# Kernel tuning notes

Hardware: AMD Instinct MI355X
Metric: run time of the kernel (lower is better)

Reference implementation:

```python
import jax, jax.numpy as jnp
import numpy as np

KSIZE = 3
RES_SCALE = 0.2
WITH_RESIDUAL = True


def setup_inputs() -> dict:
    key = jax.random.key(0)
    x = jax.random.normal(key, (8, 3, 1024, 1024), dtype=jnp.float32)
    return {"x": x}


def reference(x) -> jnp.ndarray:
    B, C, H, W = x.shape
    k = KSIZE
    p = k // 2
    # zero padding matches F.unfold(padding=k//2)
    xp = jnp.pad(x, ((0, 0), (0, 0), (p, p), (p, p)))
    # [B, C, k*k, H, W] stack of shifted views (k*k = 9, small static loop)
    patches = jnp.stack(
        [xp[:, :, di:di + H, dj:dj + W] for di in range(k) for dj in range(k)],
        axis=2,
    )
    # median of odd-sized window = middle element of sorted values
    med = jnp.sort(patches, axis=2)[:, :, (k * k) // 2]
    if WITH_RESIDUAL:
        return x + RES_SCALE * (med - x)
    return med
```

## Files before the change

kernel.cpp:

```cpp
#include <hip/hip_runtime.h>


#define S2(a, b) { float _t = fminf(a, b); b = fmaxf(a, b); a = _t; }

__device__ __forceinline__ float med3f(float a, float b, float c) {
    return fmaxf(fminf(a, b), fminf(fmaxf(a, b), c));
}

constexpr int ROWS = 16;

__global__ __launch_bounds__(256) void median_blur_kernel(
    const float* __restrict__ xin, float* __restrict__ out)
{
    const int W = 1024, H = 1024;
    const int tx   = threadIdx.x;
    const int lane = tx & 63;
    const int x0   = tx << 2;
    const int y0   = blockIdx.x * ROWS;
    const int z    = blockIdx.y;
    const size_t plane = (size_t)z * H * W;
    const float* base  = xin + plane;
    float*       obase = out + plane;

    float t[6], m[6], b[6];

    auto load_row = [&](int y, float* dst) {
        if (y < 0 || y >= H) {
#pragma unroll
            for (int j = 0; j < 6; ++j) dst[j] = 0.0f;
            return;
        }
        const float* row = base + (size_t)y * W;
        float4 c = *reinterpret_cast<const float4*>(row + x0);
        float left  = __shfl_up(c.w, 1);
        float right = __shfl_down(c.x, 1);
        if (lane == 0)  left  = (x0 > 0)     ? row[x0 - 1] : 0.0f;
        if (lane == 63) right = (x0 + 4 < W) ? row[x0 + 4] : 0.0f;
        dst[0] = left; dst[1] = c.x; dst[2] = c.y; dst[3] = c.z; dst[4] = c.w; dst[5] = right;
    };

    load_row(y0 - 1, t);
    load_row(y0,     m);
    load_row(y0 + 1, b);

#pragma unroll 4
    for (int r = 0; r < ROWS; ++r) {
        float nxt[6];
        {
            const int yn = (r < ROWS - 1) ? (y0 + r + 2) : H;
            load_row(yn, nxt);
        }

        float lo[6], mi[6], hi[6];
#pragma unroll
        for (int j = 0; j < 6; ++j) {
            float a = t[j], c0 = m[j], d = b[j];
            S2(a, c0); S2(c0, d); S2(a, c0);
            lo[j] = a; mi[j] = c0; hi[j] = d;
        }

        float4 o; float* op = &o.x;
#pragma unroll
        for (int j = 0; j < 4; ++j) {
            float mxlo = fmaxf(lo[j], fmaxf(lo[j + 1], lo[j + 2]));
            float mnhi = fminf(hi[j], fminf(hi[j + 1], hi[j + 2]));
            float mdmi = med3f(mi[j], mi[j + 1], mi[j + 2]);
            float med  = med3f(mxlo, mdmi, mnhi);
            float xc   = m[j + 1];
            op[j] = xc + 0.2f * (med - xc);
        }
        *reinterpret_cast<float4*>(obase + (size_t)(y0 + r) * W + x0) = o;

#pragma unroll
        for (int j = 0; j < 6; ++j) { t[j] = m[j]; m[j] = b[j]; b[j] = nxt[j]; }
    }
}

extern "C" void kernel_launch(void* const* d_in, const int* in_sizes, int n_in,
                              void* d_out, int out_size, void* d_ws, size_t ws_size,
                              hipStream_t stream) {
    const float* x = (const float*)d_in[0];
    float* out = (float*)d_out;
    const int H = 1024, W = 1024;
    const int planes = in_sizes[0] / (H * W);
    dim3 block(256);
    dim3 grid(H / ROWS, planes);
    median_blur_kernel<<<grid, block, 0, stream>>>(x, out);
}
```

Measured before the change: 182.1 us.

## Deepen row prefetch and load halo columns directly instead of shuffles

Raises the row prefetch distance from one to three rows ahead, keeping five rows in registers and fully unrolling the row loop. The left and right halo columns are now loaded directly from global memory (clamped and zero-masked), replacing the wavefront shuffles. Launch bounds now request four blocks per multiprocessor. The aim is to hide more memory latency in a bandwidth-bound stencil, at the cost of extra registers and redundant cached halo loads.

```diff
diff --git a/kernel.cpp b/kernel.cpp
--- a/kernel.cpp
+++ b/kernel.cpp
@@ -9,52 +9,58 @@
 
 constexpr int ROWS = 16;
 
-__global__ __launch_bounds__(256) void median_blur_kernel(
+struct Row { float v[6]; };
+
+__global__ __launch_bounds__(256, 4) void median_blur_kernel(
     const float* __restrict__ xin, float* __restrict__ out)
 {
     const int W = 1024, H = 1024;
-    const int tx   = threadIdx.x;
-    const int lane = tx & 63;
-    const int x0   = tx << 2;
-    const int y0   = blockIdx.x * ROWS;
-    const int z    = blockIdx.y;
-    const size_t plane = (size_t)z * H * W;
+    const int tx = threadIdx.x;
+    const int x0 = tx << 2;
+    const int y0 = blockIdx.x * ROWS;
+    const size_t plane = (size_t)blockIdx.y * H * W;
     const float* base  = xin + plane;
     float*       obase = out + plane;
 
-    float t[6], m[6], b[6];
+    const int  xl = (x0 > 0)     ? x0 - 1 : 0;
+    const int  xr = (x0 + 4 < W) ? x0 + 4 : W - 1;
+    const bool lz = (x0 == 0);
+    const bool rz = (x0 + 4 >= W);
 
-    auto load_row = [&](int y, float* dst) {
-        if (y < 0 || y >= H) {
+    auto load_row = [&](int y, Row& d) {
+        if ((unsigned)y < (unsigned)H) {
+            const float* row = base + (size_t)y * W;
+            const float4 c = *reinterpret_cast<const float4*>(row + x0);
+            const float  l = row[xl];
+            const float  r = row[xr];
+            d.v[0] = lz ? 0.0f : l;
+            d.v[1] = c.x; d.v[2] = c.y; d.v[3] = c.z; d.v[4] = c.w;
+            d.v[5] = rz ? 0.0f : r;
+        } else {
 #pragma unroll
-            for (int j = 0; j < 6; ++j) dst[j] = 0.0f;
-            return;
+            for (int j = 0; j < 6; ++j) d.v[j] = 0.0f;
         }
-        const float* row = base + (size_t)y * W;
-        float4 c = *reinterpret_cast<const float4*>(row + x0);
-        float left  = __shfl_up(c.w, 1);
-        float right = __shfl_down(c.x, 1);
-        if (lane == 0)  left  = (x0 > 0)     ? row[x0 - 1] : 0.0f;
-        if (lane == 63) right = (x0 + 4 < W) ? row[x0 + 4] : 0.0f;
-        dst[0] = left; dst[1] = c.x; dst[2] = c.y; dst[3] = c.z; dst[4] = c.w; dst[5] = right;
     };
 
+    Row t, m, b, p0, p1;
     load_row(y0 - 1, t);
     load_row(y0,     m);
     load_row(y0 + 1, b);
+    load_row(y0 + 2, p0);
+    load_row(y0 + 3, p1);
 
-#pragma unroll 4
+#pragma unroll
     for (int r = 0; r < ROWS; ++r) {
-        float nxt[6];
+        Row nx;
         {
-            const int yn = (r < ROWS - 1) ? (y0 + r + 2) : H;
-            load_row(yn, nxt);
+            const int yn = (r <= ROWS - 4) ? (y0 + r + 4) : H;
+            load_row(yn, nx);
         }
 
         float lo[6], mi[6], hi[6];
 #pragma unroll
         for (int j = 0; j < 6; ++j) {
-            float a = t[j], c0 = m[j], d = b[j];
+            float a = t.v[j], c0 = m.v[j], d = b.v[j];
             S2(a, c0); S2(c0, d); S2(a, c0);
             lo[j] = a; mi[j] = c0; hi[j] = d;
         }
@@ -66,13 +72,12 @@
             float mnhi = fminf(hi[j], fminf(hi[j + 1], hi[j + 2]));
             float mdmi = med3f(mi[j], mi[j + 1], mi[j + 2]);
             float med  = med3f(mxlo, mdmi, mnhi);
-            float xc   = m[j + 1];
+            float xc   = m.v[j + 1];
             op[j] = xc + 0.2f * (med - xc);
         }
         *reinterpret_cast<float4*>(obase + (size_t)(y0 + r) * W + x0) = o;
 
-#pragma unroll
-        for (int j = 0; j < 6; ++j) { t[j] = m[j]; m[j] = b[j]; b[j] = nxt[j]; }
+        t = m; m = b; b = p0; p0 = p1; p1 = nx;
     }
 }
 
```

After: 182.3 us. Within noise of the previous version (+0.1%).

## Preload all rows up front, share wave edges via LDS, nontemporal stores

Applied to the files above, without the earlier changes.

The kernel now issues all ten row loads of an 8-row tile at once, with clamped addresses and an asm barrier that keeps them in flight together, instead of streaming one row per iteration. Halo pixels at wave boundaries come from shared memory written by the edge lanes, replacing scalar global loads. Output goes through nontemporal stores, and the tile height drops from 16 to 8 with a doubled grid. The aim is more memory-level parallelism and fewer stray uncoalesced loads. The cost is more rows re-read per tile, higher register pressure, and a block-wide barrier.

```diff
diff --git a/kernel.cpp b/kernel.cpp
--- a/kernel.cpp
+++ b/kernel.cpp
@@ -1,78 +1,97 @@
 #include <hip/hip_runtime.h>
 
 
-#define S2(a, b) { float _t = fminf(a, b); b = fmaxf(a, b); a = _t; }
+typedef float v4f __attribute__((ext_vector_type(4)));
 
-__device__ __forceinline__ float med3f(float a, float b, float c) {
-    return fmaxf(fminf(a, b), fminf(fmaxf(a, b), c));
+#define S2(a,b) { float _t=fminf(a,b); (b)=fmaxf(a,b); (a)=_t; }
+__device__ __forceinline__ float med3f(float a,float b,float c){
+    return fmaxf(fminf(a,b), fminf(fmaxf(a,b),c));
 }
 
-constexpr int ROWS = 16;
+constexpr int W = 1024, H = 1024;
+constexpr int R = 8;
+constexpr int NL = R + 2;
 
-__global__ __launch_bounds__(256) void median_blur_kernel(
+__global__ __launch_bounds__(256, 2) void median_blur_kernel(
     const float* __restrict__ xin, float* __restrict__ out)
 {
-    const int W = 1024, H = 1024;
+    __shared__ float eL[NL][4];
+    __shared__ float eR[NL][4];
+
     const int tx   = threadIdx.x;
     const int lane = tx & 63;
+    const int wv   = tx >> 6;
     const int x0   = tx << 2;
-    const int y0   = blockIdx.x * ROWS;
-    const int z    = blockIdx.y;
-    const size_t plane = (size_t)z * H * W;
+    const int y0   = blockIdx.x * R;
+    const size_t plane = (size_t)blockIdx.y * H * W;
     const float* base  = xin + plane;
     float*       obase = out + plane;
 
-    float t[6], m[6], b[6];
+    v4f row[NL];
+#pragma unroll
+    for (int s = 0; s < NL; ++s) {
+        int y = y0 - 1 + s;
+        y = y < 0 ? 0 : (y > H - 1 ? H - 1 : y);
+        row[s] = *reinterpret_cast<const v4f*>(base + (size_t)y * W + x0);
+    }
+    {
+        float* rf = reinterpret_cast<float*>(row);
+#pragma unroll
+        for (int i = 0; i < NL * 4; ++i) asm volatile("" : "+v"(rf[i]));
+    }
 
-    auto load_row = [&](int y, float* dst) {
-        if (y < 0 || y >= H) {
+    if (lane == 0) {
 #pragma unroll
-            for (int j = 0; j < 6; ++j) dst[j] = 0.0f;
-            return;
-        }
-        const float* row = base + (size_t)y * W;
-        float4 c = *reinterpret_cast<const float4*>(row + x0);
-        float left  = __shfl_up(c.w, 1);
-        float right = __shfl_down(c.x, 1);
-        if (lane == 0)  left  = (x0 > 0)     ? row[x0 - 1] : 0.0f;
-        if (lane == 63) right = (x0 + 4 < W) ? row[x0 + 4] : 0.0f;
-        dst[0] = left; dst[1] = c.x; dst[2] = c.y; dst[3] = c.z; dst[4] = c.w; dst[5] = right;
-    };
+        for (int s = 0; s < NL; ++s) eL[s][wv] = row[s].x;
+    }
+    if (lane == 63) {
+#pragma unroll
+        for (int s = 0; s < NL; ++s) eR[s][wv] = row[s].w;
+    }
+    __syncthreads();
 
-    load_row(y0 - 1, t);
-    load_row(y0,     m);
-    load_row(y0 + 1, b);
+    float rr[NL][6];
+#pragma unroll
+    for (int s = 0; s < NL; ++s) {
+        const int y = y0 - 1 + s;
+        const bool valid = (y >= 0) && (y < H);
+        v4f c = row[s];
+        float l = __shfl_up(c.w, 1);
+        float r = __shfl_down(c.x, 1);
+        if (lane == 0)  l = (wv > 0) ? eR[s][wv - 1] : 0.0f;
+        if (lane == 63) r = (wv < 3) ? eL[s][wv + 1] : 0.0f;
+        rr[s][0] = valid ? l   : 0.0f;
+        rr[s][1] = valid ? c.x : 0.0f;
+        rr[s][2] = valid ? c.y : 0.0f;
+        rr[s][3] = valid ? c.z : 0.0f;
+        rr[s][4] = valid ? c.w : 0.0f;
+        rr[s][5] = valid ? r   : 0.0f;
+    }
 
-#pragma unroll 4
-    for (int r = 0; r < ROWS; ++r) {
-        float nxt[6];
-        {
-            const int yn = (r < ROWS - 1) ? (y0 + r + 2) : H;
-            load_row(yn, nxt);
-        }
-
+#pragma unroll
+    for (int r = 0; r < R; ++r) {
+        const float* t  = rr[r];
+        const float* mm = rr[r + 1];
+        const float* bb = rr[r + 2];
         float lo[6], mi[6], hi[6];
 #pragma unroll
         for (int j = 0; j < 6; ++j) {
-            float a = t[j], c0 = m[j], d = b[j];
+            float a = t[j], c0 = mm[j], d = bb[j];
             S2(a, c0); S2(c0, d); S2(a, c0);
             lo[j] = a; mi[j] = c0; hi[j] = d;
         }
-
-        float4 o; float* op = &o.x;
+        v4f o;
 #pragma unroll
         for (int j = 0; j < 4; ++j) {
             float mxlo = fmaxf(lo[j], fmaxf(lo[j + 1], lo[j + 2]));
             float mnhi = fminf(hi[j], fminf(hi[j + 1], hi[j + 2]));
             float mdmi = med3f(mi[j], mi[j + 1], mi[j + 2]);
             float med  = med3f(mxlo, mdmi, mnhi);
-            float xc   = m[j + 1];
-            op[j] = xc + 0.2f * (med - xc);
+            float xc   = mm[j + 1];
+            o[j] = xc + 0.2f * (med - xc);
         }
-        *reinterpret_cast<float4*>(obase + (size_t)(y0 + r) * W + x0) = o;
-
-#pragma unroll
-        for (int j = 0; j < 6; ++j) { t[j] = m[j]; m[j] = b[j]; b[j] = nxt[j]; }
+        __builtin_nontemporal_store(o,
+            reinterpret_cast<v4f*>(obase + (size_t)(y0 + r) * W + x0));
     }
 }
 
@@ -81,9 +100,8 @@
                               hipStream_t stream) {
     const float* x = (const float*)d_in[0];
     float* out = (float*)d_out;
-    const int H = 1024, W = 1024;
     const int planes = in_sizes[0] / (H * W);
     dim3 block(256);
-    dim3 grid(H / ROWS, planes);
+    dim3 grid(H / R, planes);
     median_blur_kernel<<<grid, block, 0, stream>>>(x, out);
 }
```

New measurement: 176.0 us. -3.3%, faster.
